# Kernel tuning notes

Hardware: AMD Instinct MI355X
Metric: run time of the kernel (lower is better)

The kernel has to match this reference:

```python
import jax, jax.numpy as jnp
import numpy as np

KLEN = 3  # kernel_len, since input_F has 9 = 3**2 channels


def local_crf(F, Q):
    """Per-pixel dynamic local filtering.
    F: [b, K*K, h, w] per-pixel kernel weights
    Q: [b, g, h, w] features
    out[b,g,i,j] = sum_k F[b,k,i,j] * Q[b,g,i+di_k,j+dj_k] (zero-padded 'same').
    """
    b, g, h, w = Q.shape
    p = KLEN // 2
    Qp = jnp.pad(Q, ((0, 0), (0, 0), (p, p), (p, p)))
    out = jnp.zeros_like(Q)
    k = 0
    for di in range(KLEN):
        for dj in range(KLEN):
            out = out + F[:, k][:, None] * Qp[:, :, di:di + h, dj:dj + w]
            k += 1
    return out


def setup_inputs() -> dict:
    key = jax.random.key(0)
    k1, k2, k3 = jax.random.split(key, 3)
    b, C, G, h, w = 4, 19, 8, 512, 512
    input_F = jax.random.uniform(k1, (b, KLEN * KLEN, h, w), dtype=jnp.float32)
    input_logit = jax.random.normal(k2, (b, C, h, w), dtype=jnp.float32)
    matrix = jax.random.uniform(k3, (G, C, 1, 1), dtype=jnp.float32, minval=-0.05, maxval=0.05)
    return {"input_F": input_F, "input_logit": input_logit, "matrix": matrix}


def reference(input_F, input_logit, matrix):
    # softmax over categories
    Q = jax.nn.softmax(input_logit, axis=1)                 # [b,C,h,w]
    # encoding matrix: softmax over groups of sharpened params; 1x1 conv == einsum
    E = jax.nn.softmax(100.0 * matrix, axis=0)[:, :, 0, 0]  # [G,C]
    Qg = jnp.einsum('gc,bchw->bghw', E, Q)                  # encode C -> G
    out = local_crf(input_F, Qg)                            # [b,G,h,w]
    out = jnp.einsum('gc,bghw->bchw', E, out)               # decode G -> C (E^T)
    return input_logit - out
```

## Files before the change

### kernel.cpp

```cpp
#include <hip/hip_runtime.h>

#define C_DIM 19
#define G_DIM 8
#define H_DIM 512
#define W_DIM 512
#define B_DIM 4
#define PLANE (H_DIM * W_DIM)
#define NT    256
#define TLX   64
#define TLY   8
#define HXX   (TLX + 2)
#define HYY   (TLY + 2)

__device__ __forceinline__ unsigned bf16rne(float f) {
    unsigned x = __float_as_uint(f);
    return (x + 0x7fffu + ((x >> 16) & 1u)) >> 16;
}
__device__ __forceinline__ float up_lo(unsigned u) { return __uint_as_float(u << 16); }
__device__ __forceinline__ float up_hi(unsigned u) { return __uint_as_float(u & 0xffff0000u); }

__device__ __forceinline__ void build_E_nosync(const float* __restrict__ matrix,
                                               float4 (*E4)[2], int tid) {
    if (tid < C_DIM) {
        const int c = tid;
        float m[G_DIM];
        float mx = -1e30f;
        #pragma unroll
        for (int g = 0; g < G_DIM; ++g) {
            m[g] = 100.0f * matrix[g * C_DIM + c];
            mx = fmaxf(mx, m[g]);
        }
        float s = 0.0f;
        #pragma unroll
        for (int g = 0; g < G_DIM; ++g) { m[g] = __expf(m[g] - mx); s += m[g]; }
        const float inv = 1.0f / s;
        E4[c][0] = make_float4(m[0]*inv, m[1]*inv, m[2]*inv, m[3]*inv);
        E4[c][1] = make_float4(m[4]*inv, m[5]*inv, m[6]*inv, m[7]*inv);
    }
}

__global__ __launch_bounds__(NT)
void gacrf_tile(const float* __restrict__ F,
                const float* __restrict__ logit,
                const float* __restrict__ matrix,
                float* __restrict__ out)
{
    __shared__ float4 E4[C_DIM][2];
    __shared__ uint4  ldsQ[HYY][HXX];

    const int tid = threadIdx.x;

    const int bid = blockIdx.x;
    const int swz = (bid & 7) * 256 + (bid >> 3);
    const int b   = swz >> 9;
    const int rem = swz & 511;
    const int tby = rem >> 3;
    const int tbx = rem & 7;
    const int x0  = tbx * TLX;
    const int y0  = tby * TLY;

    const int tx = tid & 31;
    const int ty = tid >> 5;
    const int gx = x0 + tx * 2;
    const int gy = y0 + ty;
    const size_t pix = (size_t)gy * W_DIM + gx;

    const float* __restrict__ logit_b = logit + (size_t)b * C_DIM * PLANE;

    const float* __restrict__ Fp = F + (size_t)b * 9 * PLANE + pix;
    float2 wk[9];
    #pragma unroll
    for (int k = 0; k < 9; ++k) wk[k] = *(const float2*)(Fp + (size_t)k * PLANE);

    build_E_nosync(matrix, E4, tid);
    __syncthreads();

    {
        const float* __restrict__ p = logit_b + pix;
        float eg[G_DIM][2];
        #pragma unroll
        for (int g = 0; g < G_DIM; ++g) { eg[g][0] = 0.0f; eg[g][1] = 0.0f; }
        float s0 = 0.0f, s1 = 0.0f;
        #pragma unroll
        for (int c = 0; c < C_DIM; ++c) {
            const float2 lv = *(const float2*)(p + (size_t)c * PLANE);
            const float e0 = __expf(lv.x);
            const float e1 = __expf(lv.y);
            s0 += e0; s1 += e1;
            const float4 E0 = E4[c][0];
            const float4 E1 = E4[c][1];
            eg[0][0] = fmaf(E0.x, e0, eg[0][0]);  eg[0][1] = fmaf(E0.x, e1, eg[0][1]);
            eg[1][0] = fmaf(E0.y, e0, eg[1][0]);  eg[1][1] = fmaf(E0.y, e1, eg[1][1]);
            eg[2][0] = fmaf(E0.z, e0, eg[2][0]);  eg[2][1] = fmaf(E0.z, e1, eg[2][1]);
            eg[3][0] = fmaf(E0.w, e0, eg[3][0]);  eg[3][1] = fmaf(E0.w, e1, eg[3][1]);
            eg[4][0] = fmaf(E1.x, e0, eg[4][0]);  eg[4][1] = fmaf(E1.x, e1, eg[4][1]);
            eg[5][0] = fmaf(E1.y, e0, eg[5][0]);  eg[5][1] = fmaf(E1.y, e1, eg[5][1]);
            eg[6][0] = fmaf(E1.z, e0, eg[6][0]);  eg[6][1] = fmaf(E1.z, e1, eg[6][1]);
            eg[7][0] = fmaf(E1.w, e0, eg[7][0]);  eg[7][1] = fmaf(E1.w, e1, eg[7][1]);
        }
        const float i0 = 1.0f / s0;
        const float i1 = 1.0f / s1;
        uint4 u0, u1;
        u0.x = bf16rne(eg[0][0]*i0) | (bf16rne(eg[1][0]*i0) << 16);
        u0.y = bf16rne(eg[2][0]*i0) | (bf16rne(eg[3][0]*i0) << 16);
        u0.z = bf16rne(eg[4][0]*i0) | (bf16rne(eg[5][0]*i0) << 16);
        u0.w = bf16rne(eg[6][0]*i0) | (bf16rne(eg[7][0]*i0) << 16);
        u1.x = bf16rne(eg[0][1]*i1) | (bf16rne(eg[1][1]*i1) << 16);
        u1.y = bf16rne(eg[2][1]*i1) | (bf16rne(eg[3][1]*i1) << 16);
        u1.z = bf16rne(eg[4][1]*i1) | (bf16rne(eg[5][1]*i1) << 16);
        u1.w = bf16rne(eg[6][1]*i1) | (bf16rne(eg[7][1]*i1) << 16);
        ldsQ[1 + ty][1 + tx * 2]     = u0;
        ldsQ[1 + ty][1 + tx * 2 + 1] = u1;
    }

    if (tid < 148) {
        int hx, hy;
        if (tid < 66)       { hx = tid;        hy = 0; }
        else if (tid < 132) { hx = tid - 66;   hy = 9; }
        else if (tid < 140) { hx = 0;          hy = 1 + (tid - 132); }
        else                { hx = 65;         hy = 1 + (tid - 140); }
        const int hgx = min(max(x0 - 1 + hx, 0), W_DIM - 1);
        const int hgy = min(max(y0 - 1 + hy, 0), H_DIM - 1);
        const float* __restrict__ p = logit_b + (size_t)hgy * W_DIM + hgx;

        float eg[G_DIM];
        #pragma unroll
        for (int g = 0; g < G_DIM; ++g) eg[g] = 0.0f;
        float s = 0.0f;
        #pragma unroll
        for (int c = 0; c < C_DIM; ++c) {
            const float e = __expf(p[(size_t)c * PLANE]);
            s += e;
            const float4 E0 = E4[c][0];
            const float4 E1 = E4[c][1];
            eg[0] = fmaf(E0.x, e, eg[0]);
            eg[1] = fmaf(E0.y, e, eg[1]);
            eg[2] = fmaf(E0.z, e, eg[2]);
            eg[3] = fmaf(E0.w, e, eg[3]);
            eg[4] = fmaf(E1.x, e, eg[4]);
            eg[5] = fmaf(E1.y, e, eg[5]);
            eg[6] = fmaf(E1.z, e, eg[6]);
            eg[7] = fmaf(E1.w, e, eg[7]);
        }
        const float inv = 1.0f / s;
        uint4 u;
        u.x = bf16rne(eg[0]*inv) | (bf16rne(eg[1]*inv) << 16);
        u.y = bf16rne(eg[2]*inv) | (bf16rne(eg[3]*inv) << 16);
        u.z = bf16rne(eg[4]*inv) | (bf16rne(eg[5]*inv) << 16);
        u.w = bf16rne(eg[6]*inv) | (bf16rne(eg[7]*inv) << 16);
        ldsQ[hy][hx] = u;
    }
    __syncthreads();

    const bool vyr[3] = { gy > 0, true, gy < H_DIM - 1 };
    const bool vxc[4] = { gx > 0, true, true, gx + 2 < W_DIM };
    const int lx = tx * 2;

    float og[G_DIM][2];
    #pragma unroll
    for (int g = 0; g < G_DIM; ++g) { og[g][0] = 0.0f; og[g][1] = 0.0f; }

    #pragma unroll
    for (int r = 0; r < 3; ++r) {
        const uint4 q0 = ldsQ[ty + r][lx];
        const uint4 q1 = ldsQ[ty + r][lx + 1];
        const uint4 q2 = ldsQ[ty + r][lx + 2];
        const uint4 q3 = ldsQ[ty + r][lx + 3];
        const uint4 qv_[4] = { q0, q1, q2, q3 };

        #pragma unroll
        for (int dxi = 0; dxi < 3; ++dxi) {
            const int k = r * 3 + dxi;
            const float wkv[2] = { wk[k].x, wk[k].y };
            #pragma unroll
            for (int j = 0; j < 2; ++j) {
                const bool v = vyr[r] & vxc[j + dxi];
                const float wv = v ? wkv[j] : 0.0f;
                const uint4 qv = qv_[j + dxi];
                og[0][j] = fmaf(wv, up_lo(qv.x), og[0][j]);
                og[1][j] = fmaf(wv, up_hi(qv.x), og[1][j]);
                og[2][j] = fmaf(wv, up_lo(qv.y), og[2][j]);
                og[3][j] = fmaf(wv, up_hi(qv.y), og[3][j]);
                og[4][j] = fmaf(wv, up_lo(qv.z), og[4][j]);
                og[5][j] = fmaf(wv, up_hi(qv.z), og[5][j]);
                og[6][j] = fmaf(wv, up_lo(qv.w), og[6][j]);
                og[7][j] = fmaf(wv, up_hi(qv.w), og[7][j]);
            }
        }
    }

    const float* __restrict__ lp = logit_b + pix;
    float* __restrict__ op = out + (size_t)b * C_DIM * PLANE + pix;
    #pragma unroll
    for (int c = 0; c < C_DIM; ++c) {
        const float2 lv = *(const float2*)(lp + (size_t)c * PLANE);
        const float4 E0 = E4[c][0];
        const float4 E1 = E4[c][1];
        float d0 = og[0][0] * E0.x;
        float d1 = og[0][1] * E0.x;
        d0 = fmaf(og[1][0], E0.y, d0);  d1 = fmaf(og[1][1], E0.y, d1);
        d0 = fmaf(og[2][0], E0.z, d0);  d1 = fmaf(og[2][1], E0.z, d1);
        d0 = fmaf(og[3][0], E0.w, d0);  d1 = fmaf(og[3][1], E0.w, d1);
        d0 = fmaf(og[4][0], E1.x, d0);  d1 = fmaf(og[4][1], E1.x, d1);
        d0 = fmaf(og[5][0], E1.y, d0);  d1 = fmaf(og[5][1], E1.y, d1);
        d0 = fmaf(og[6][0], E1.z, d0);  d1 = fmaf(og[6][1], E1.z, d1);
        d0 = fmaf(og[7][0], E1.w, d0);  d1 = fmaf(og[7][1], E1.w, d1);
        float2 o;
        o.x = lv.x - d0;
        o.y = lv.y - d1;
        *(float2*)(op + (size_t)c * PLANE) = o;
    }
}

extern "C" void kernel_launch(void* const* d_in, const int* in_sizes, int n_in,
                              void* d_out, int out_size, void* d_ws, size_t ws_size,
                              hipStream_t stream) {
    const float* F      = (const float*)d_in[0];
    const float* logit  = (const float*)d_in[1];
    const float* matrix = (const float*)d_in[2];
    float* out = (float*)d_out;

    gacrf_tile<<<2048, NT, 0, stream>>>(F, logit, matrix, out);
}
```

Baseline: 51.15 us.

## Use one pixel per thread with 512 threads and cache logits as bf16 in LDS

Doubles the block to 512 threads so each thread handles one pixel instead of two. The logits are stashed in shared memory as bf16 on their first read, so the final output pass no longer re-reads 19 planes from global memory. F weights are now loaded late, per row, instead of up front. The aim is to cut global traffic and register pressure. In exchange, the output is built from bf16-rounded logits, which loses precision in the `input_logit - out` term. The change also adds about 19 KB of LDS per block, which may reduce occupancy.

```diff
diff --git a/kernel.cpp b/kernel.cpp
--- a/kernel.cpp
+++ b/kernel.cpp
@@ -6,7 +6,7 @@
 #define W_DIM 512
 #define B_DIM 4
 #define PLANE (H_DIM * W_DIM)
-#define NT    256
+#define NT    512
 #define TLX   64
 #define TLY   8
 #define HXX   (TLX + 2)
@@ -45,8 +45,9 @@
                 const float* __restrict__ matrix,
                 float* __restrict__ out)
 {
-    __shared__ float4 E4[C_DIM][2];
-    __shared__ uint4  ldsQ[HYY][HXX];
+    __shared__ float4         E4[C_DIM][2];
+    __shared__ uint4          ldsQ[HYY][HXX];
+    __shared__ unsigned short ldsL[C_DIM][NT];
 
     const int tid = threadIdx.x;
 
@@ -59,58 +60,47 @@
     const int x0  = tbx * TLX;
     const int y0  = tby * TLY;
 
-    const int tx = tid & 31;
-    const int ty = tid >> 5;
-    const int gx = x0 + tx * 2;
+    const int tx = tid & 63;
+    const int ty = tid >> 6;
+    const int gx = x0 + tx;
     const int gy = y0 + ty;
     const size_t pix = (size_t)gy * W_DIM + gx;
 
     const float* __restrict__ logit_b = logit + (size_t)b * C_DIM * PLANE;
 
-    const float* __restrict__ Fp = F + (size_t)b * 9 * PLANE + pix;
-    float2 wk[9];
-    #pragma unroll
-    for (int k = 0; k < 9; ++k) wk[k] = *(const float2*)(Fp + (size_t)k * PLANE);
-
     build_E_nosync(matrix, E4, tid);
     __syncthreads();
 
     {
         const float* __restrict__ p = logit_b + pix;
-        float eg[G_DIM][2];
-        #pragma unroll
-        for (int g = 0; g < G_DIM; ++g) { eg[g][0] = 0.0f; eg[g][1] = 0.0f; }
-        float s0 = 0.0f, s1 = 0.0f;
+        float eg[G_DIM];
+        #pragma unroll
+        for (int g = 0; g < G_DIM; ++g) eg[g] = 0.0f;
+        float s = 0.0f;
         #pragma unroll
         for (int c = 0; c < C_DIM; ++c) {
-            const float2 lv = *(const float2*)(p + (size_t)c * PLANE);
-            const float e0 = __expf(lv.x);
-            const float e1 = __expf(lv.y);
-            s0 += e0; s1 += e1;
+            const float lv = p[(size_t)c * PLANE];
+            ldsL[c][tid] = (unsigned short)bf16rne(lv);
+            const float e = __expf(lv);
+            s += e;
             const float4 E0 = E4[c][0];
             const float4 E1 = E4[c][1];
-            eg[0][0] = fmaf(E0.x, e0, eg[0][0]);  eg[0][1] = fmaf(E0.x, e1, eg[0][1]);
-            eg[1][0] = fmaf(E0.y, e0, eg[1][0]);  eg[1][1] = fmaf(E0.y, e1, eg[1][1]);
-            eg[2][0] = fmaf(E0.z, e0, eg[2][0]);  eg[2][1] = fmaf(E0.z, e1, eg[2][1]);
-            eg[3][0] = fmaf(E0.w, e0, eg[3][0]);  eg[3][1] = fmaf(E0.w, e1, eg[3][1]);
-            eg[4][0] = fmaf(E1.x, e0, eg[4][0]);  eg[4][1] = fmaf(E1.x, e1, eg[4][1]);
-            eg[5][0] = fmaf(E1.y, e0, eg[5][0]);  eg[5][1] = fmaf(E1.y, e1, eg[5][1]);
-            eg[6][0] = fmaf(E1.z, e0, eg[6][0]);  eg[6][1] = fmaf(E1.z, e1, eg[6][1]);
-            eg[7][0] = fmaf(E1.w, e0, eg[7][0]);  eg[7][1] = fmaf(E1.w, e1, eg[7][1]);
-        }
-        const float i0 = 1.0f / s0;
-        const float i1 = 1.0f / s1;
-        uint4 u0, u1;
-        u0.x = bf16rne(eg[0][0]*i0) | (bf16rne(eg[1][0]*i0) << 16);
-        u0.y = bf16rne(eg[2][0]*i0) | (bf16rne(eg[3][0]*i0) << 16);
-        u0.z = bf16rne(eg[4][0]*i0) | (bf16rne(eg[5][0]*i0) << 16);
-        u0.w = bf16rne(eg[6][0]*i0) | (bf16rne(eg[7][0]*i0) << 16);
-        u1.x = bf16rne(eg[0][1]*i1) | (bf16rne(eg[1][1]*i1) << 16);
-        u1.y = bf16rne(eg[2][1]*i1) | (bf16rne(eg[3][1]*i1) << 16);
-        u1.z = bf16rne(eg[4][1]*i1) | (bf16rne(eg[5][1]*i1) << 16);
-        u1.w = bf16rne(eg[6][1]*i1) | (bf16rne(eg[7][1]*i1) << 16);
-        ldsQ[1 + ty][1 + tx * 2]     = u0;
-        ldsQ[1 + ty][1 + tx * 2 + 1] = u1;
+            eg[0] = fmaf(E0.x, e, eg[0]);
+            eg[1] = fmaf(E0.y, e, eg[1]);
+            eg[2] = fmaf(E0.z, e, eg[2]);
+            eg[3] = fmaf(E0.w, e, eg[3]);
+            eg[4] = fmaf(E1.x, e, eg[4]);
+            eg[5] = fmaf(E1.y, e, eg[5]);
+            eg[6] = fmaf(E1.z, e, eg[6]);
+            eg[7] = fmaf(E1.w, e, eg[7]);
+        }
+        const float inv = 1.0f / s;
+        uint4 u;
+        u.x = bf16rne(eg[0]*inv) | (bf16rne(eg[1]*inv) << 16);
+        u.y = bf16rne(eg[2]*inv) | (bf16rne(eg[3]*inv) << 16);
+        u.z = bf16rne(eg[4]*inv) | (bf16rne(eg[5]*inv) << 16);
+        u.w = bf16rne(eg[6]*inv) | (bf16rne(eg[7]*inv) << 16);
+        ldsQ[1 + ty][1 + tx] = u;
     }
 
     if (tid < 148) {
@@ -153,62 +143,55 @@
     __syncthreads();
 
     const bool vyr[3] = { gy > 0, true, gy < H_DIM - 1 };
-    const bool vxc[4] = { gx > 0, true, true, gx + 2 < W_DIM };
-    const int lx = tx * 2;
-
-    float og[G_DIM][2];
+    const bool vxc[3] = { gx > 0, true, gx < W_DIM - 1 };
+    const float* __restrict__ Fp = F + (size_t)b * 9 * PLANE + pix;
+
+    float og[G_DIM];
     #pragma unroll
-    for (int g = 0; g < G_DIM; ++g) { og[g][0] = 0.0f; og[g][1] = 0.0f; }
+    for (int g = 0; g < G_DIM; ++g) og[g] = 0.0f;
 
     #pragma unroll
     for (int r = 0; r < 3; ++r) {
-        const uint4 q0 = ldsQ[ty + r][lx];
-        const uint4 q1 = ldsQ[ty + r][lx + 1];
-        const uint4 q2 = ldsQ[ty + r][lx + 2];
-        const uint4 q3 = ldsQ[ty + r][lx + 3];
-        const uint4 qv_[4] = { q0, q1, q2, q3 };
+        const float w0 = Fp[(size_t)(r * 3 + 0) * PLANE];
+        const float w1 = Fp[(size_t)(r * 3 + 1) * PLANE];
+        const float w2 = Fp[(size_t)(r * 3 + 2) * PLANE];
+        const float wr[3] = { w0, w1, w2 };
+
+        const uint4 qa = ldsQ[ty + r][tx];
+        const uint4 qb = ldsQ[ty + r][tx + 1];
+        const uint4 qc = ldsQ[ty + r][tx + 2];
+        const uint4 qv_[3] = { qa, qb, qc };
 
         #pragma unroll
         for (int dxi = 0; dxi < 3; ++dxi) {
-            const int k = r * 3 + dxi;
-            const float wkv[2] = { wk[k].x, wk[k].y };
-            #pragma unroll
-            for (int j = 0; j < 2; ++j) {
-                const bool v = vyr[r] & vxc[j + dxi];
-                const float wv = v ? wkv[j] : 0.0f;
-                const uint4 qv = qv_[j + dxi];
-                og[0][j] = fmaf(wv, up_lo(qv.x), og[0][j]);
-                og[1][j] = fmaf(wv, up_hi(qv.x), og[1][j]);
-                og[2][j] = fmaf(wv, up_lo(qv.y), og[2][j]);
-                og[3][j] = fmaf(wv, up_hi(qv.y), og[3][j]);
-                og[4][j] = fmaf(wv, up_lo(qv.z), og[4][j]);
-                og[5][j] = fmaf(wv, up_hi(qv.z), og[5][j]);
-                og[6][j] = fmaf(wv, up_lo(qv.w), og[6][j]);
-                og[7][j] = fmaf(wv, up_hi(qv.w), og[7][j]);
-            }
-        }
-    }
-
-    const float* __restrict__ lp = logit_b + pix;
+            const float wv = (vyr[r] & vxc[dxi]) ? wr[dxi] : 0.0f;
+            const uint4 qv = qv_[dxi];
+            og[0] = fmaf(wv, up_lo(qv.x), og[0]);
+            og[1] = fmaf(wv, up_hi(qv.x), og[1]);
+            og[2] = fmaf(wv, up_lo(qv.y), og[2]);
+            og[3] = fmaf(wv, up_hi(qv.y), og[3]);
+            og[4] = fmaf(wv, up_lo(qv.z), og[4]);
+            og[5] = fmaf(wv, up_hi(qv.z), og[5]);
+            og[6] = fmaf(wv, up_lo(qv.w), og[6]);
+            og[7] = fmaf(wv, up_hi(qv.w), og[7]);
+        }
+    }
+
     float* __restrict__ op = out + (size_t)b * C_DIM * PLANE + pix;
     #pragma unroll
     for (int c = 0; c < C_DIM; ++c) {
-        const float2 lv = *(const float2*)(lp + (size_t)c * PLANE);
+        const float lv = up_lo((unsigned)ldsL[c][tid]);
         const float4 E0 = E4[c][0];
         const float4 E1 = E4[c][1];
-        float d0 = og[0][0] * E0.x;
-        float d1 = og[0][1] * E0.x;
-        d0 = fmaf(og[1][0], E0.y, d0);  d1 = fmaf(og[1][1], E0.y, d1);
-        d0 = fmaf(og[2][0], E0.z, d0);  d1 = fmaf(og[2][1], E0.z, d1);
-        d0 = fmaf(og[3][0], E0.w, d0);  d1 = fmaf(og[3][1], E0.w, d1);
-        d0 = fmaf(og[4][0], E1.x, d0);  d1 = fmaf(og[4][1], E1.x, d1);
-        d0 = fmaf(og[5][0], E1.y, d0);  d1 = fmaf(og[5][1], E1.y, d1);
-        d0 = fmaf(og[6][0], E1.z, d0);  d1 = fmaf(og[6][1], E1.z, d1);
-        d0 = fmaf(og[7][0], E1.w, d0);  d1 = fmaf(og[7][1], E1.w, d1);
-        float2 o;
-        o.x = lv.x - d0;
-        o.y = lv.y - d1;
-        *(float2*)(op + (size_t)c * PLANE) = o;
+        float d = og[0] * E0.x;
+        d = fmaf(og[1], E0.y, d);
+        d = fmaf(og[2], E0.z, d);
+        d = fmaf(og[3], E0.w, d);
+        d = fmaf(og[4], E1.x, d);
+        d = fmaf(og[5], E1.y, d);
+        d = fmaf(og[6], E1.z, d);
+        d = fmaf(og[7], E1.w, d);
+        op[(size_t)c * PLANE] = lv - d;
     }
 }
 
```

New measurement: 46.39 us. 9.3% less time.
